# Performance work log

Measured on AMD Instinct MI355X. Metric: run time of the kernel, lower is better.

The kernel has to match this reference:

```python
import jax, jax.numpy as jnp
import numpy as np

VOCAB = 32000
ROUTE_BIAS = 10.0  # weight on the deterministic one-hot route vs mu logits


def setup_inputs() -> dict:
    key = jax.random.key(0)
    k1, k2, k3, k4, k5, k6 = jax.random.split(key, 6)
    B, S, H = 2, 4096, 1024
    E, Ie = 8, 512  # intermediate_size=4096 -> expert_intermediate=512, fused dim=2*Ie=1024
    return {
        "hidden_states": jax.random.normal(k1, (B, S, H), dtype=jnp.float32),
        "token_ids": jax.random.randint(k2, (B, S), 0, VOCAB),
        "mu": jax.random.normal(k3, (B, S, H), dtype=jnp.float32),
        "gate_up_proj": jax.random.normal(k4, (E, H, 2 * Ie), dtype=jnp.float32) * 0.02,
        "down_proj": jax.random.normal(k5, (E, Ie, H), dtype=jnp.float32) * 0.02,
        "mu_router_w": jax.random.normal(k6, (E, H), dtype=jnp.float32) * 0.02,
    }


def reference(hidden_states, token_ids, mu, gate_up_proj, down_proj, mu_router_w):
    B, S, H = hidden_states.shape
    E, _, F2 = gate_up_proj.shape
    Ie = F2 // 2
    N = B * S

    # deterministic token->expert routing, optionally perturbed by mu logits
    token_to_expert = jnp.arange(VOCAB, dtype=jnp.int32) % E
    base_expert = token_to_expert[jnp.clip(token_ids, 0, VOCAB - 1)]      # [B,S]
    mu_logits = jnp.einsum('bsh,eh->bse', mu, mu_router_w)                 # [B,S,E]
    combined = jax.nn.one_hot(base_expert, E, dtype=mu_logits.dtype) * ROUTE_BIAS + mu_logits
    expert_ids = jnp.argmax(combined, axis=-1).reshape(N)                  # [N]

    x = hidden_states.reshape(N, H)
    tok = jnp.arange(N)

    # compute per-expert GEMM then select per-token expert output
    # (same math as gathering the full weight slab per token, without the
    #  N*H*2Ie gathered-weight blowup of the original torch code)
    gu_all = jnp.einsum('nh,ehf->enf', x, gate_up_proj)                    # [E,N,2Ie]
    gu = gu_all[expert_ids, tok]                                           # [N,2Ie]
    gate, up = gu[:, :Ie], gu[:, Ie:]
    inter = jax.nn.silu(gate) * up                                         # [N,Ie]

    z_all = jnp.einsum('ni,eih->enh', inter, down_proj)                    # [E,N,H]
    out = z_all[expert_ids, tok].reshape(B, S, H)
    return out
```

## Files before the change

kernel.cpp:

```cpp
#include <hip/hip_runtime.h>
#include <hip/hip_bf16.h>
#include <stdint.h>

typedef __bf16 bf16x8 __attribute__((ext_vector_type(8)));
typedef float f32x4 __attribute__((ext_vector_type(4)));

#define ROUTE_BIAS_F 10.0f
#define VOCAB_SZ 32000

__device__ __forceinline__ unsigned short f2bf(float f) {
    union { float f; unsigned u; } v; v.f = f;
    unsigned u = v.u;
    unsigned r = u + 0x7FFFu + ((u >> 16) & 1u);
    return (unsigned short)(r >> 16);
}
__device__ __forceinline__ float bf2f(unsigned short s) {
    union { unsigned u; float f; } v; v.u = ((unsigned)s) << 16;
    return v.f;
}
__device__ __forceinline__ void ld16(const unsigned short* g, unsigned short* l) {
    __builtin_amdgcn_global_load_lds(
        (const __attribute__((address_space(1))) void*)g,
        (__attribute__((address_space(3))) void*)l, 16, 0, 0);
}

__global__ void k_convert_bf16(const float* __restrict__ in,
                               unsigned short* __restrict__ out, int n) {
    int i = (blockIdx.x * blockDim.x + threadIdx.x) * 4;
    if (i + 3 < n) {
        float4 f = *(const float4*)(in + i);
        ushort4 o;
        o.x = f2bf(f.x); o.y = f2bf(f.y); o.z = f2bf(f.z); o.w = f2bf(f.w);
        *(ushort4*)(out + i) = o;
    } else {
        for (; i < n; ++i) out[i] = f2bf(in[i]);
    }
}

__global__ void k_transpose_bf16(const float* __restrict__ in,
                                 unsigned short* __restrict__ out, int R, int C) {
    __shared__ float tile[32][33];
    int e = blockIdx.z;
    const float* inp = in + (size_t)e * R * C;
    unsigned short* outp = out + (size_t)e * R * C;
    int c0 = blockIdx.x * 32, r0 = blockIdx.y * 32;
    int tx = threadIdx.x, ty = threadIdx.y;
#pragma unroll
    for (int k = 0; k < 32; k += 8)
        tile[ty + k][tx] = inp[(size_t)(r0 + ty + k) * C + c0 + tx];
    __syncthreads();
#pragma unroll
    for (int k = 0; k < 32; k += 8)
        outp[(size_t)(c0 + ty + k) * R + r0 + tx] = f2bf(tile[tx][ty + k]);
}

__global__ void k_logits(const float* __restrict__ mu, const int* __restrict__ tok_ids,
                         const float* __restrict__ rw, int H, int N,
                         int* __restrict__ eids) {
    int lane = threadIdx.x & 63;
    int wv   = threadIdx.x >> 6;
    int tok  = blockIdx.x * 4 + wv;
    if (tok >= N) return;
    float acc[8];
#pragma unroll
    for (int e = 0; e < 8; ++e) acc[e] = 0.f;
    const float* m = mu + (size_t)tok * H;
    for (int h = lane; h < H; h += 64) {
        float mv = m[h];
#pragma unroll
        for (int e = 0; e < 8; ++e) acc[e] += mv * rw[e * H + h];
    }
#pragma unroll
    for (int e = 0; e < 8; ++e) {
        float v = acc[e];
#pragma unroll
        for (int off = 32; off > 0; off >>= 1) v += __shfl_xor(v, off);
        acc[e] = v;
    }
    if (lane == 0) {
        int t = tok_ids[tok];
        if (t < 0) t = 0;
        if (t > VOCAB_SZ - 1) t = VOCAB_SZ - 1;
        int be = t % 8;
        float best = -1e30f; int bi = 0;
#pragma unroll
        for (int e = 0; e < 8; ++e) {
            float v = acc[e] + (e == be ? ROUTE_BIAS_F : 0.f);
            if (v > best) { best = v; bi = e; }
        }
        eids[tok] = bi;
    }
}

__global__ void k_count(const int* __restrict__ eids,
                        int* __restrict__ blockcnt, int N) {
    __shared__ int cnt[8];
    int tid = threadIdx.x;
    if (tid < 8) cnt[tid] = 0;
    __syncthreads();
    int tok = blockIdx.x * 256 + tid;
    int lane = tid & 63;
    int eid = (tok < N) ? eids[tok] : -1;
#pragma unroll
    for (int e = 0; e < 8; ++e) {
        unsigned long long m = __ballot(eid == e);
        if (lane == 0 && m) atomicAdd(&cnt[e], __popcll(m));
    }
    __syncthreads();
    if (tid < 8) blockcnt[blockIdx.x * 8 + tid] = cnt[tid];
}

__global__ void k_scan(const int* __restrict__ blockcnt,
                       int* __restrict__ counts, int* __restrict__ base_,
                       int* __restrict__ offs, int NB) {
    __shared__ int tot[8];
    int lane = threadIdx.x;
    int e = lane >> 3, g = lane & 7;
    int v[4];
    int s = 0;
#pragma unroll
    for (int i = 0; i < 4; ++i) { v[i] = s; s += blockcnt[(g * 4 + i) * 8 + e]; }
    int inc = s;
#pragma unroll
    for (int d = 1; d < 8; d <<= 1) {
        int t = __shfl_up(inc, d);
        if (g >= d) inc += t;
    }
    int excl = inc - s;
#pragma unroll
    for (int i = 0; i < 4; ++i) offs[(g * 4 + i) * 8 + e] = excl + v[i];
    if (g == 7) { counts[e] = inc; tot[e] = inc; }
    __syncthreads();
    if (lane == 0) {
        int s2 = 0;
#pragma unroll
        for (int i = 0; i < 8; ++i) { base_[i] = s2; s2 += tot[i]; }
    }
}

__global__ void k_scatter(const int* __restrict__ eids,
                          const int* __restrict__ offs,
                          int* __restrict__ list, int N) {
    __shared__ int wavecnt[4][8];
    int tid = threadIdx.x;
    int lane = tid & 63, wv = tid >> 6;
    int tok = blockIdx.x * 256 + tid;
    int eid = (tok < N) ? eids[tok] : -1;
    unsigned long long below = (1ull << lane) - 1ull;
    int myrank = 0;
#pragma unroll
    for (int e = 0; e < 8; ++e) {
        unsigned long long m = __ballot(eid == e);
        if (lane == 0) wavecnt[wv][e] = __popcll(m);
        if (eid == e) myrank = __popcll(m & below);
    }
    __syncthreads();
    if (eid >= 0) {
        int pre = 0;
        for (int w = 0; w < wv; ++w) pre += wavecnt[w][eid];
        int pos = offs[blockIdx.x * 8 + eid] + pre + myrank;
        list[eid * N + pos] = tok;
    }
}

#define TM 128
#define TN 128
#define TK 64

__global__ __launch_bounds__(256, 2) void k_gemm_gateup(
    const unsigned short* __restrict__ X,
    const unsigned short* __restrict__ Wt,
    unsigned short* __restrict__ GU,
    const int* __restrict__ counts, const int* __restrict__ base_,
    const int* __restrict__ list, int N, int H, int F2) {
    int e = blockIdx.z, mt = blockIdx.y, nt = blockIdx.x;
    int cnt = counts[e];
    int m0 = mt * TM;
    if (m0 >= cnt) return;
    int n0 = nt * TN;

    __shared__ __align__(16) unsigned short As[TM * TK];
    __shared__ __align__(16) unsigned short Bs[TN * TK];

    int tid = threadIdx.x;
    int lane = tid & 63, wv = tid >> 6;
    int wm = (wv >> 1) * 64, wn = (wv & 1) * 64;

    int rowg = lane >> 3;
    int sl   = (lane & 7) ^ rowg;

    const unsigned short* We = Wt + ((size_t)e * F2 + n0) * H;
    const unsigned short* ag[4];
    const unsigned short* bg[4];
#pragma unroll
    for (int i = 0; i < 4; ++i) {
        int r = wv * 32 + i * 8 + rowg;
        int gr = m0 + r;
        int tokrow = (gr < cnt) ? list[e * N + gr] : 0;
        ag[i] = X + (size_t)tokrow * H + sl * 8;
        bg[i] = We + (size_t)r * H + sl * 8;
    }

    f32x4 acc[4][4];
#pragma unroll
    for (int i = 0; i < 4; ++i)
#pragma unroll
        for (int j = 0; j < 4; ++j) acc[i][j] = (f32x4)(0.f);

    int q = lane >> 4, m = lane & 15;
    int sw = m & 7;

    for (int k0 = 0; k0 < H; k0 += TK) {
#pragma unroll
        for (int i = 0; i < 4; ++i)
            ld16(ag[i] + k0, &As[(wv * 32 + i * 8) * TK]);
#pragma unroll
        for (int i = 0; i < 4; ++i)
            ld16(bg[i] + k0, &Bs[(wv * 32 + i * 8) * TK]);
        __syncthreads();
#pragma unroll
        for (int ks = 0; ks < TK; ks += 32) {
            int kc = ks >> 3;
            int ck = ((kc + q) ^ sw) << 3;
            bf16x8 af[4], bfr[4];
#pragma unroll
            for (int im = 0; im < 4; ++im)
                af[im] = *(const bf16x8*)&As[(wm + m + im * 16) * TK + ck];
#pragma unroll
            for (int in_ = 0; in_ < 4; ++in_)
                bfr[in_] = *(const bf16x8*)&Bs[(wn + m + in_ * 16) * TK + ck];
#pragma unroll
            for (int im = 0; im < 4; ++im)
#pragma unroll
                for (int in_ = 0; in_ < 4; ++in_)
                    acc[im][in_] = __builtin_amdgcn_mfma_f32_16x16x32_bf16(
                        af[im], bfr[in_], acc[im][in_], 0, 0, 0);
        }
        __syncthreads();
    }

    int b = base_[e];
#pragma unroll
    for (int im = 0; im < 4; ++im) {
#pragma unroll
        for (int j = 0; j < 4; ++j) {
            int row = wm + im * 16 + (lane >> 4) * 4 + j;
            int gr = m0 + row;
            if (gr < cnt) {
                unsigned short* orow = GU + (size_t)(b + gr) * F2 + n0;
#pragma unroll
                for (int in_ = 0; in_ < 4; ++in_) {
                    int col = wn + in_ * 16 + (lane & 15);
                    orow[col] = f2bf(acc[im][in_][j]);
                }
            }
        }
    }
}

__global__ void k_silu(const unsigned short* __restrict__ GU,
                       unsigned short* __restrict__ IT, int N, int Ie) {
    int idx = blockIdx.x * blockDim.x + threadIdx.x;
    int total = (N * Ie) >> 3;
    if (idx >= total) return;
    int per_row = Ie >> 3;
    int r = idx / per_row, c = (idx - r * per_row) * 8;
    const unsigned short* g8 = GU + (size_t)r * 2 * Ie + c;
    const unsigned short* u8 = g8 + Ie;
    ushort4 ga = *(const ushort4*)g8, gb = *(const ushort4*)(g8 + 4);
    ushort4 ua = *(const ushort4*)u8, ub = *(const ushort4*)(u8 + 4);
    unsigned short o[8];
    unsigned short gs[8] = {ga.x, ga.y, ga.z, ga.w, gb.x, gb.y, gb.z, gb.w};
    unsigned short us[8] = {ua.x, ua.y, ua.z, ua.w, ub.x, ub.y, ub.z, ub.w};
#pragma unroll
    for (int i = 0; i < 8; ++i) {
        float g = bf2f(gs[i]), u = bf2f(us[i]);
        float s = g / (1.f + __expf(-g));
        o[i] = f2bf(s * u);
    }
    ushort4 oa = {o[0], o[1], o[2], o[3]}, ob = {o[4], o[5], o[6], o[7]};
    unsigned short* op = IT + (size_t)r * Ie + c;
    *(ushort4*)op = oa;
    *(ushort4*)(op + 4) = ob;
}

__global__ __launch_bounds__(256, 2) void k_gemm_down(
    const unsigned short* __restrict__ IT,
    const unsigned short* __restrict__ Wt,
    float* __restrict__ OUT,
    const int* __restrict__ counts, const int* __restrict__ base_,
    const int* __restrict__ list, int N, int Ie, int H) {
    int e = blockIdx.z, mt = blockIdx.y, nt = blockIdx.x;
    int cnt = counts[e];
    int m0 = mt * TM;
    if (m0 >= cnt) return;
    int n0 = nt * TN;
    int b = base_[e];

    __shared__ __align__(16) unsigned short As[TM * TK];
    __shared__ __align__(16) unsigned short Bs[TN * TK];

    int tid = threadIdx.x;
    int lane = tid & 63, wv = tid >> 6;
    int wm = (wv >> 1) * 64, wn = (wv & 1) * 64;

    int rowg = lane >> 3;
    int sl   = (lane & 7) ^ rowg;

    const unsigned short* We = Wt + ((size_t)e * H + n0) * Ie;
    const unsigned short* ag[4];
    const unsigned short* bg[4];
#pragma unroll
    for (int i = 0; i < 4; ++i) {
        int r = wv * 32 + i * 8 + rowg;
        int gr = m0 + r;
        int arow = (gr < cnt) ? (b + gr) : b;
        ag[i] = IT + (size_t)arow * Ie + sl * 8;
        bg[i] = We + (size_t)r * Ie + sl * 8;
    }

    f32x4 acc[4][4];
#pragma unroll
    for (int i = 0; i < 4; ++i)
#pragma unroll
        for (int j = 0; j < 4; ++j) acc[i][j] = (f32x4)(0.f);

    int q = lane >> 4, m = lane & 15;
    int sw = m & 7;

    for (int k0 = 0; k0 < Ie; k0 += TK) {
#pragma unroll
        for (int i = 0; i < 4; ++i)
            ld16(ag[i] + k0, &As[(wv * 32 + i * 8) * TK]);
#pragma unroll
        for (int i = 0; i < 4; ++i)
            ld16(bg[i] + k0, &Bs[(wv * 32 + i * 8) * TK]);
        __syncthreads();
#pragma unroll
        for (int ks = 0; ks < TK; ks += 32) {
            int kc = ks >> 3;
            int ck = ((kc + q) ^ sw) << 3;
            bf16x8 af[4], bfr[4];
#pragma unroll
            for (int im = 0; im < 4; ++im)
                af[im] = *(const bf16x8*)&As[(wm + m + im * 16) * TK + ck];
#pragma unroll
            for (int in_ = 0; in_ < 4; ++in_)
                bfr[in_] = *(const bf16x8*)&Bs[(wn + m + in_ * 16) * TK + ck];
#pragma unroll
            for (int im = 0; im < 4; ++im)
#pragma unroll
                for (int in_ = 0; in_ < 4; ++in_)
                    acc[im][in_] = __builtin_amdgcn_mfma_f32_16x16x32_bf16(
                        af[im], bfr[in_], acc[im][in_], 0, 0, 0);
        }
        __syncthreads();
    }

#pragma unroll
    for (int im = 0; im < 4; ++im) {
#pragma unroll
        for (int j = 0; j < 4; ++j) {
            int row = wm + im * 16 + (lane >> 4) * 4 + j;
            int gr = m0 + row;
            if (gr < cnt) {
                int tok = list[e * N + gr];
                float* orow = OUT + (size_t)tok * H + n0;
#pragma unroll
                for (int in_ = 0; in_ < 4; ++in_) {
                    int col = wn + in_ * 16 + (lane & 15);
                    orow[col] = acc[im][in_][j];
                }
            }
        }
    }
}

extern "C" void kernel_launch(void* const* d_in, const int* in_sizes, int n_in,
                              void* d_out, int out_size, void* d_ws, size_t ws_size,
                              hipStream_t stream) {
    const float* hidden   = (const float*)d_in[0];
    const int*   tok_ids  = (const int*)d_in[1];
    const float* mu       = (const float*)d_in[2];
    const float* gup      = (const float*)d_in[3];
    const float* dnp      = (const float*)d_in[4];
    const float* rw       = (const float*)d_in[5];
    float* out = (float*)d_out;

    int N  = in_sizes[1];
    int H  = in_sizes[0] / N;
    int E  = in_sizes[5] / H;
    int F2 = in_sizes[3] / (E * H);
    int Ie = F2 / 2;

    int NB = (N + 255) / 256;

    char* ws = (char*)d_ws;
    size_t o = 0;
    auto alloc = [&](size_t sz) {
        size_t r = o;
        o += (sz + 255) & ~(size_t)255;
        return r;
    };
    int* counts   = (int*)(ws + alloc((size_t)E * 4));
    int* base_    = (int*)(ws + alloc((size_t)E * 4));
    int* eids     = (int*)(ws + alloc((size_t)N * 4));
    int* blockcnt = (int*)(ws + alloc((size_t)NB * 8 * 4));
    int* offs     = (int*)(ws + alloc((size_t)NB * 8 * 4));
    int* list     = (int*)(ws + alloc((size_t)E * N * 4));
    unsigned short* xb   = (unsigned short*)(ws + alloc((size_t)N * H * 2));
    unsigned short* wgut = (unsigned short*)(ws + alloc((size_t)E * F2 * H * 2));
    unsigned short* wdnt = (unsigned short*)(ws + alloc((size_t)E * H * Ie * 2));
    unsigned short* gu   = (unsigned short*)(ws + alloc((size_t)N * F2 * 2));
    unsigned short* inter = xb;

    k_convert_bf16<<<dim3((N * H / 4 + 255) / 256), dim3(256), 0, stream>>>(hidden, xb, N * H);

    dim3 tb(32, 8);
    k_transpose_bf16<<<dim3(F2 / 32, H / 32, E), tb, 0, stream>>>(gup, wgut, H, F2);
    k_transpose_bf16<<<dim3(H / 32, Ie / 32, E), tb, 0, stream>>>(dnp, wdnt, Ie, H);

    k_logits<<<dim3((N + 3) / 4), dim3(256), 0, stream>>>(mu, tok_ids, rw, H, N, eids);
    k_count<<<dim3(NB), dim3(256), 0, stream>>>(eids, blockcnt, N);
    k_scan<<<dim3(1), dim3(64), 0, stream>>>(blockcnt, counts, base_, offs, NB);
    k_scatter<<<dim3(NB), dim3(256), 0, stream>>>(eids, offs, list, N);

    dim3 g1(F2 / TN, (N + TM - 1) / TM, E);
    k_gemm_gateup<<<g1, dim3(256), 0, stream>>>(xb, wgut, gu, counts, base_, list, N, H, F2);

    k_silu<<<dim3((N * Ie / 8 + 255) / 256), dim3(256), 0, stream>>>(gu, inter, N, Ie);

    dim3 g2(H / TN, (N + TM - 1) / TM, E);
    k_gemm_down<<<g2, dim3(256), 0, stream>>>(inter, wdnt, out, counts, base_, list, N, Ie, H);
}
```

Baseline: 245.1 us.

## Fuse SiLU into gate-up GEMM epilogue, double-buffer LDS, flatten grid

The gate-up GEMM now loads interleaved gate/up weight rows, so adjacent output columns hold the gate and up values for the same index. The epilogue combines them with a lane shuffle, applies SiLU, and writes the intermediate directly, which removes the separate SiLU kernel and the round trip of the full gate-up buffer. Both GEMMs now double-buffer their LDS tiles to overlap the next K-tile load with MFMA work, at the cost of twice the shared memory. The grid is flattened with the expert index in the low bits so blocks of different experts interleave, which may affect occupancy and cache behaviour.

```diff
diff --git a/kernel.cpp b/kernel.cpp
--- a/kernel.cpp
+++ b/kernel.cpp
@@ -170,17 +170,21 @@
 __global__ __launch_bounds__(256, 2) void k_gemm_gateup(
     const unsigned short* __restrict__ X,
     const unsigned short* __restrict__ Wt,
-    unsigned short* __restrict__ GU,
+    unsigned short* __restrict__ IT,
     const int* __restrict__ counts, const int* __restrict__ base_,
-    const int* __restrict__ list, int N, int H, int F2) {
-    int e = blockIdx.z, mt = blockIdx.y, nt = blockIdx.x;
+    const int* __restrict__ list, int N, int H, int Ie) {
+    int bid = blockIdx.x;
+    int e = bid & 7;
+    int t = bid >> 3;
+    int nt = t & 7;
+    int mt = t >> 3;
     int cnt = counts[e];
     int m0 = mt * TM;
     if (m0 >= cnt) return;
-    int n0 = nt * TN;
-
-    __shared__ __align__(16) unsigned short As[TM * TK];
-    __shared__ __align__(16) unsigned short Bs[TN * TK];
+    int F2 = 2 * Ie;
+
+    __shared__ __align__(16) unsigned short As[2][TM * TK];
+    __shared__ __align__(16) unsigned short Bs[2][TN * TK];
 
     int tid = threadIdx.x;
     int lane = tid & 63, wv = tid >> 6;
@@ -189,7 +193,6 @@
     int rowg = lane >> 3;
     int sl   = (lane & 7) ^ rowg;
 
-    const unsigned short* We = Wt + ((size_t)e * F2 + n0) * H;
     const unsigned short* ag[4];
     const unsigned short* bg[4];
 #pragma unroll
@@ -198,7 +201,8 @@
         int gr = m0 + r;
         int tokrow = (gr < cnt) ? list[e * N + gr] : 0;
         ag[i] = X + (size_t)tokrow * H + sl * 8;
-        bg[i] = We + (size_t)r * H + sl * 8;
+        int wrow = (r & 1) * Ie + nt * 64 + (r >> 1);
+        bg[i] = Wt + ((size_t)e * F2 + wrow) * H + sl * 8;
     }
 
     f32x4 acc[4][4];
@@ -210,14 +214,22 @@
     int q = lane >> 4, m = lane & 15;
     int sw = m & 7;
 
-    for (int k0 = 0; k0 < H; k0 += TK) {
-#pragma unroll
-        for (int i = 0; i < 4; ++i)
-            ld16(ag[i] + k0, &As[(wv * 32 + i * 8) * TK]);
-#pragma unroll
-        for (int i = 0; i < 4; ++i)
-            ld16(bg[i] + k0, &Bs[(wv * 32 + i * 8) * TK]);
+#pragma unroll
+    for (int i = 0; i < 4; ++i) ld16(ag[i], &As[0][(wv * 32 + i * 8) * TK]);
+#pragma unroll
+    for (int i = 0; i < 4; ++i) ld16(bg[i], &Bs[0][(wv * 32 + i * 8) * TK]);
+
+    int NKI = H / TK;
+    int p = 0;
+    for (int ki = 0; ki < NKI; ++ki, p ^= 1) {
         __syncthreads();
+        if (ki + 1 < NKI) {
+            int kn = (ki + 1) * TK;
+#pragma unroll
+            for (int i = 0; i < 4; ++i) ld16(ag[i] + kn, &As[p ^ 1][(wv * 32 + i * 8) * TK]);
+#pragma unroll
+            for (int i = 0; i < 4; ++i) ld16(bg[i] + kn, &Bs[p ^ 1][(wv * 32 + i * 8) * TK]);
+        }
 #pragma unroll
         for (int ks = 0; ks < TK; ks += 32) {
             int kc = ks >> 3;
@@ -225,10 +237,10 @@
             bf16x8 af[4], bfr[4];
 #pragma unroll
             for (int im = 0; im < 4; ++im)
-                af[im] = *(const bf16x8*)&As[(wm + m + im * 16) * TK + ck];
+                af[im] = *(const bf16x8*)&As[p][(wm + m + im * 16) * TK + ck];
 #pragma unroll
             for (int in_ = 0; in_ < 4; ++in_)
-                bfr[in_] = *(const bf16x8*)&Bs[(wn + m + in_ * 16) * TK + ck];
+                bfr[in_] = *(const bf16x8*)&Bs[p][(wn + m + in_ * 16) * TK + ck];
 #pragma unroll
             for (int im = 0; im < 4; ++im)
 #pragma unroll
@@ -236,52 +248,30 @@
                     acc[im][in_] = __builtin_amdgcn_mfma_f32_16x16x32_bf16(
                         af[im], bfr[in_], acc[im][in_], 0, 0, 0);
         }
-        __syncthreads();
     }
 
     int b = base_[e];
+    int nt64 = nt * 64;
 #pragma unroll
     for (int im = 0; im < 4; ++im) {
 #pragma unroll
         for (int j = 0; j < 4; ++j) {
-            int row = wm + im * 16 + (lane >> 4) * 4 + j;
+            int row = wm + im * 16 + q * 4 + j;
             int gr = m0 + row;
-            if (gr < cnt) {
-                unsigned short* orow = GU + (size_t)(b + gr) * F2 + n0;
-#pragma unroll
-                for (int in_ = 0; in_ < 4; ++in_) {
-                    int col = wn + in_ * 16 + (lane & 15);
-                    orow[col] = f2bf(acc[im][in_][j]);
+#pragma unroll
+            for (int in_ = 0; in_ < 4; ++in_) {
+                float v = acc[im][in_][j];
+                float u = __shfl_xor(v, 1);
+                float g = v;
+                float s = g / (1.f + __expf(-g));
+                float res = s * u;
+                if (!(lane & 1) && gr < cnt) {
+                    int oc = nt64 + ((wn + in_ * 16 + m) >> 1);
+                    IT[(size_t)(b + gr) * Ie + oc] = f2bf(res);
                 }
             }
         }
     }
-}
-
-__global__ void k_silu(const unsigned short* __restrict__ GU,
-                       unsigned short* __restrict__ IT, int N, int Ie) {
-    int idx = blockIdx.x * blockDim.x + threadIdx.x;
-    int total = (N * Ie) >> 3;
-    if (idx >= total) return;
-    int per_row = Ie >> 3;
-    int r = idx / per_row, c = (idx - r * per_row) * 8;
-    const unsigned short* g8 = GU + (size_t)r * 2 * Ie + c;
-    const unsigned short* u8 = g8 + Ie;
-    ushort4 ga = *(const ushort4*)g8, gb = *(const ushort4*)(g8 + 4);
-    ushort4 ua = *(const ushort4*)u8, ub = *(const ushort4*)(u8 + 4);
-    unsigned short o[8];
-    unsigned short gs[8] = {ga.x, ga.y, ga.z, ga.w, gb.x, gb.y, gb.z, gb.w};
-    unsigned short us[8] = {ua.x, ua.y, ua.z, ua.w, ub.x, ub.y, ub.z, ub.w};
-#pragma unroll
-    for (int i = 0; i < 8; ++i) {
-        float g = bf2f(gs[i]), u = bf2f(us[i]);
-        float s = g / (1.f + __expf(-g));
-        o[i] = f2bf(s * u);
-    }
-    ushort4 oa = {o[0], o[1], o[2], o[3]}, ob = {o[4], o[5], o[6], o[7]};
-    unsigned short* op = IT + (size_t)r * Ie + c;
-    *(ushort4*)op = oa;
-    *(ushort4*)(op + 4) = ob;
 }
 
 __global__ __launch_bounds__(256, 2) void k_gemm_down(
@@ -290,15 +280,19 @@
     float* __restrict__ OUT,
     const int* __restrict__ counts, const int* __restrict__ base_,
     const int* __restrict__ list, int N, int Ie, int H) {
-    int e = blockIdx.z, mt = blockIdx.y, nt = blockIdx.x;
+    int bid = blockIdx.x;
+    int e = bid & 7;
+    int t = bid >> 3;
+    int nt = t & 7;
+    int mt = t >> 3;
     int cnt = counts[e];
     int m0 = mt * TM;
     if (m0 >= cnt) return;
     int n0 = nt * TN;
     int b = base_[e];
 
-    __shared__ __align__(16) unsigned short As[TM * TK];
-    __shared__ __align__(16) unsigned short Bs[TN * TK];
+    __shared__ __align__(16) unsigned short As[2][TM * TK];
+    __shared__ __align__(16) unsigned short Bs[2][TN * TK];
 
     int tid = threadIdx.x;
     int lane = tid & 63, wv = tid >> 6;
@@ -328,14 +322,22 @@
     int q = lane >> 4, m = lane & 15;
     int sw = m & 7;
 
-    for (int k0 = 0; k0 < Ie; k0 += TK) {
-#pragma unroll
-        for (int i = 0; i < 4; ++i)
-            ld16(ag[i] + k0, &As[(wv * 32 + i * 8) * TK]);
-#pragma unroll
-        for (int i = 0; i < 4; ++i)
-            ld16(bg[i] + k0, &Bs[(wv * 32 + i * 8) * TK]);
+#pragma unroll
+    for (int i = 0; i < 4; ++i) ld16(ag[i], &As[0][(wv * 32 + i * 8) * TK]);
+#pragma unroll
+    for (int i = 0; i < 4; ++i) ld16(bg[i], &Bs[0][(wv * 32 + i * 8) * TK]);
+
+    int NKI = Ie / TK;
+    int p = 0;
+    for (int ki = 0; ki < NKI; ++ki, p ^= 1) {
         __syncthreads();
+        if (ki + 1 < NKI) {
+            int kn = (ki + 1) * TK;
+#pragma unroll
+            for (int i = 0; i < 4; ++i) ld16(ag[i] + kn, &As[p ^ 1][(wv * 32 + i * 8) * TK]);
+#pragma unroll
+            for (int i = 0; i < 4; ++i) ld16(bg[i] + kn, &Bs[p ^ 1][(wv * 32 + i * 8) * TK]);
+        }
 #pragma unroll
         for (int ks = 0; ks < TK; ks += 32) {
             int kc = ks >> 3;
@@ -343,10 +345,10 @@
             bf16x8 af[4], bfr[4];
 #pragma unroll
             for (int im = 0; im < 4; ++im)
-                af[im] = *(const bf16x8*)&As[(wm + m + im * 16) * TK + ck];
+                af[im] = *(const bf16x8*)&As[p][(wm + m + im * 16) * TK + ck];
 #pragma unroll
             for (int in_ = 0; in_ < 4; ++in_)
-                bfr[in_] = *(const bf16x8*)&Bs[(wn + m + in_ * 16) * TK + ck];
+                bfr[in_] = *(const bf16x8*)&Bs[p][(wn + m + in_ * 16) * TK + ck];
 #pragma unroll
             for (int im = 0; im < 4; ++im)
 #pragma unroll
@@ -354,21 +356,20 @@
                     acc[im][in_] = __builtin_amdgcn_mfma_f32_16x16x32_bf16(
                         af[im], bfr[in_], acc[im][in_], 0, 0, 0);
         }
-        __syncthreads();
     }
 
 #pragma unroll
     for (int im = 0; im < 4; ++im) {
 #pragma unroll
         for (int j = 0; j < 4; ++j) {
-            int row = wm + im * 16 + (lane >> 4) * 4 + j;
+            int row = wm + im * 16 + q * 4 + j;
             int gr = m0 + row;
             if (gr < cnt) {
                 int tok = list[e * N + gr];
                 float* orow = OUT + (size_t)tok * H + n0;
 #pragma unroll
                 for (int in_ = 0; in_ < 4; ++in_) {
-                    int col = wn + in_ * 16 + (lane & 15);
+                    int col = wn + in_ * 16 + m;
                     orow[col] = acc[im][in_][j];
                 }
             }
@@ -411,8 +412,7 @@
     unsigned short* xb   = (unsigned short*)(ws + alloc((size_t)N * H * 2));
     unsigned short* wgut = (unsigned short*)(ws + alloc((size_t)E * F2 * H * 2));
     unsigned short* wdnt = (unsigned short*)(ws + alloc((size_t)E * H * Ie * 2));
-    unsigned short* gu   = (unsigned short*)(ws + alloc((size_t)N * F2 * 2));
-    unsigned short* inter = xb;
+    unsigned short* it   = (unsigned short*)(ws + alloc((size_t)N * Ie * 2));
 
     k_convert_bf16<<<dim3((N * H / 4 + 255) / 256), dim3(256), 0, stream>>>(hidden, xb, N * H);
 
@@ -425,11 +425,10 @@
     k_scan<<<dim3(1), dim3(64), 0, stream>>>(blockcnt, counts, base_, offs, NB);
     k_scatter<<<dim3(NB), dim3(256), 0, stream>>>(eids, offs, list, N);
 
-    dim3 g1(F2 / TN, (N + TM - 1) / TM, E);
-    k_gemm_gateup<<<g1, dim3(256), 0, stream>>>(xb, wgut, gu, counts, base_, list, N, H, F2);
-
-    k_silu<<<dim3((N * Ie / 8 + 255) / 256), dim3(256), 0, stream>>>(gu, inter, N, Ie);
-
-    dim3 g2(H / TN, (N + TM - 1) / TM, E);
-    k_gemm_down<<<g2, dim3(256), 0, stream>>>(inter, wdnt, out, counts, base_, list, N, Ie, H);
-}
+    int MT = (N + TM - 1) / TM;
+    k_gemm_gateup<<<dim3(E * MT * (Ie / 64)), dim3(256), 0, stream>>>(
+        xb, wgut, it, counts, base_, list, N, H, Ie);
+
+    k_gemm_down<<<dim3(E * MT * (H / TN)), dim3(256), 0, stream>>>(
+        it, wdnt, out, counts, base_, list, N, Ie, H);
+}
```

Result: faster. 240.0 us (-2.1%).
